# Performance work log

Measured on AMD Instinct MI355X. Metric: run time of the kernel, lower is better.

The kernel has to match this reference:

```python
import jax, jax.numpy as jnp
import numpy as np

D_MODEL = 2048
N_HEAD = 16
D_K = D_MODEL // N_HEAD  # 128
B, S = 2, 2048


def setup_inputs() -> dict:
    key = jax.random.key(0)
    ks = jax.random.split(key, 10)
    std = 1.0 / np.sqrt(D_MODEL)
    inp = {
        "x": jax.random.normal(ks[0], (B, S, D_MODEL), dtype=jnp.float32),
        "mask": jnp.ones((B, 1, S, S), dtype=jnp.int32),
        # Linear weights stored as [in, out] for x @ W + b
        "w_q": jax.random.normal(ks[1], (D_MODEL, D_MODEL), dtype=jnp.float32) * std,
        "b_q": jnp.zeros((D_MODEL,), dtype=jnp.float32),
        "w_k": jax.random.normal(ks[2], (D_MODEL, D_K), dtype=jnp.float32) * std,
        "b_k": jnp.zeros((D_K,), dtype=jnp.float32),
        "w_v": jax.random.normal(ks[3], (D_MODEL, D_K), dtype=jnp.float32) * std,
        "b_v": jnp.zeros((D_K,), dtype=jnp.float32),
        "w_o": jax.random.normal(ks[4], (D_MODEL, D_MODEL), dtype=jnp.float32) * std,
        "b_o": jnp.zeros((D_MODEL,), dtype=jnp.float32),
    }
    return inp


def reference(x, mask, w_q, b_q, w_k, b_k, w_v, b_v, w_o, b_o):
    b, s, _ = x.shape
    # Q: [b, h, s, d_k]; K/V single shared head: [b, 1, s, d_k]
    q = (x @ w_q + b_q).reshape(b, s, N_HEAD, D_K).transpose(0, 2, 1, 3)
    k = (x @ w_k + b_k)[:, None, :, :]
    v = (x @ w_v + b_v)[:, None, :, :]
    scale = jnp.sqrt(jnp.float32(D_K))
    # scores: [b, h, s, s] (K head broadcast over h)
    scores = jnp.einsum("bhqd,bzkd->bhqk", q, k) / scale
    scores = jnp.where(mask == 0, jnp.float32(-jnp.inf), scores)
    attn = jax.nn.softmax(scores, axis=-1)
    out = jnp.einsum("bhqk,bzkd->bhqd", attn, v)  # [b, h, s, d_k]
    out = out.transpose(0, 2, 1, 3).reshape(b, s, D_MODEL)
    return out @ w_o + b_o
```

## Files before the change

### kernel.cpp

```cpp
#include <hip/hip_runtime.h>

typedef __attribute__((ext_vector_type(8))) short bf16x8;
typedef __attribute__((ext_vector_type(4))) float f32x4;

#define GLD_LDS16(g, l)                                                        \
  __builtin_amdgcn_global_load_lds(                                            \
      (const __attribute__((address_space(1))) void*)(g),                      \
      (__attribute__((address_space(3))) void*)(l), 16, 0, 0)

__device__ __forceinline__ f32x4 mfma_bf16(bf16x8 a, bf16x8 b, f32x4 c) {
  return __builtin_amdgcn_mfma_f32_16x16x32_bf16(a, b, c, 0, 0, 0);
}

__device__ __forceinline__ unsigned short f2bf(float f) {
  union { float f; unsigned int u; } a;
  a.f = f;
  unsigned int u = a.u;
  unsigned int r = (u + 0x7fffu + ((u >> 16) & 1u)) >> 16;
  return (unsigned short)r;
}


__global__ void k_convert(const float* __restrict__ in,
                          unsigned short* __restrict__ out, int n8) {
  int i = blockIdx.x * 256 + threadIdx.x;
  if (i >= n8) return;
  const float4* p = reinterpret_cast<const float4*>(in) + (size_t)i * 2;
  float4 a = p[0], b = p[1];
  union { unsigned short u[8]; uint4 v; } pk;
  pk.u[0] = f2bf(a.x); pk.u[1] = f2bf(a.y); pk.u[2] = f2bf(a.z); pk.u[3] = f2bf(a.w);
  pk.u[4] = f2bf(b.x); pk.u[5] = f2bf(b.y); pk.u[6] = f2bf(b.z); pk.u[7] = f2bf(b.w);
  reinterpret_cast<uint4*>(out)[i] = pk.v;
}

__global__ void k_transpose(const float* __restrict__ in,
                            unsigned short* __restrict__ out, int R, int C) {
  __shared__ float tile[32][33];
  int c0 = blockIdx.x * 32, r0 = blockIdx.y * 32;
  int tx = threadIdx.x, ty = threadIdx.y;
#pragma unroll
  for (int j = 0; j < 4; ++j)
    tile[ty + j * 8][tx] = in[(size_t)(r0 + ty + j * 8) * C + (c0 + tx)];
  __syncthreads();
#pragma unroll
  for (int j = 0; j < 4; ++j)
    out[(size_t)(c0 + ty + j * 8) * R + (r0 + tx)] = f2bf(tile[tx][ty + j * 8]);
}

__global__ void k_bias_concat(const float* __restrict__ bq,
                              const float* __restrict__ bk,
                              const float* __restrict__ bv,
                              float* __restrict__ o) {
  int i = blockIdx.x * 256 + threadIdx.x;
  if (i < 2048) o[i] = bq[i];
  else if (i < 2176) o[i] = bk[i - 2048];
  else if (i < 2304) o[i] = bv[i - 2176];
}


template <bool OUT_F32>
__global__ __launch_bounds__(256, 2) void k_gemm(
    const unsigned short* __restrict__ A, const unsigned short* __restrict__ Bt,
    const float* __restrict__ bias, void* __restrict__ Cp, int M, int N, int K) {
  __shared__ __align__(16) unsigned short lda[128 * 32];
  __shared__ __align__(16) unsigned short ldb[128 * 32];
  const int t = threadIdx.x;
  const int l = t & 63;
  const int w = t >> 6;
  const int wr = w >> 1, wc = w & 1;
  const int lr = l & 15, lg = l >> 4;
  const int m0 = blockIdx.y * 128, n0 = blockIdx.x * 128;

  f32x4 acc[4][4] = {};

  for (int kt = 0; kt < K; kt += 32) {
#pragma unroll
    for (int c = 0; c < 2; ++c) {
      int idx = t * 8 + c * 2048;
      int row = idx >> 5, col = idx & 31;
      GLD_LDS16(A + (size_t)(m0 + row) * K + kt + col, lda + w * 512 + c * 2048);
      GLD_LDS16(Bt + (size_t)(n0 + row) * K + kt + col, ldb + w * 512 + c * 2048);
    }
    __syncthreads();
    bf16x8 af[4], bfr[4];
#pragma unroll
    for (int i = 0; i < 4; ++i)
      af[i] = *reinterpret_cast<const bf16x8*>(lda + (wr * 64 + i * 16 + lr) * 32 + lg * 8);
#pragma unroll
    for (int j = 0; j < 4; ++j)
      bfr[j] = *reinterpret_cast<const bf16x8*>(ldb + (wc * 64 + j * 16 + lr) * 32 + lg * 8);
#pragma unroll
    for (int i = 0; i < 4; ++i)
#pragma unroll
      for (int j = 0; j < 4; ++j)
        acc[i][j] = mfma_bf16(af[i], bfr[j], acc[i][j]);
    __syncthreads();
  }

#pragma unroll
  for (int j = 0; j < 4; ++j) {
    int col = n0 + wc * 64 + j * 16 + lr;
    float bv = bias[col];
#pragma unroll
    for (int i = 0; i < 4; ++i) {
      int rowb = m0 + wr * 64 + i * 16 + lg * 4;
#pragma unroll
      for (int r = 0; r < 4; ++r) {
        float v = acc[i][j][r] + bv;
        if (OUT_F32)
          reinterpret_cast<float*>(Cp)[(size_t)(rowb + r) * N + col] = v;
        else
          reinterpret_cast<unsigned short*>(Cp)[(size_t)(rowb + r) * N + col] = f2bf(v);
      }
    }
  }
}


__global__ __launch_bounds__(512, 4) void k_attn(
    const unsigned short* __restrict__ qkv, unsigned short* __restrict__ out) {
  __shared__ __align__(16) unsigned short k_lds[2][64 * 128];
  __shared__ __align__(16) unsigned short v_lds[128 * 68];
  __shared__ __align__(16) unsigned short p_lds[128 * 72];

  const int t = threadIdx.x, l = t & 63, w = t >> 6;
  const int lr = l & 15, lg = l >> 4;
  const int bid = blockIdx.x;
  const int qt = bid & 15, h = (bid >> 4) & 15, b = bid >> 8;
  const size_t rowQ0 = (size_t)b * 2048 + qt * 128;
  const size_t rowK0 = (size_t)b * 2048;

  bf16x8 qf[4];
  {
    const unsigned short* qrow = qkv + (rowQ0 + w * 16 + lr) * 2304 + h * 128;
#pragma unroll
    for (int kd = 0; kd < 4; ++kd)
      qf[kd] = *reinterpret_cast<const bf16x8*>(qrow + kd * 32 + lg * 8);
  }

#pragma unroll
  for (int c = 0; c < 2; ++c) {
    int f16 = t + c * 512;
    int row = f16 >> 4;
    int col16 = (f16 & 15) ^ (row & 7);
    GLD_LDS16(qkv + (rowK0 + row) * 2304 + 2048 + col16 * 8,
              &k_lds[0][0] + w * 512 + c * 4096);
  }
  bf16x8 vst[2];
#pragma unroll
  for (int c = 0; c < 2; ++c)
    vst[c] = *reinterpret_cast<const bf16x8*>(
        qkv + (rowK0 + l) * 2304 + 2176 + w * 16 + c * 8);
#pragma unroll
  for (int c = 0; c < 2; ++c)
#pragma unroll
    for (int e = 0; e < 8; ++e)
      v_lds[(w * 16 + c * 8 + e) * 68 + l] = (unsigned short)vst[c][e];
  __syncthreads();

  f32x4 o_acc[8] = {};
  float m_s = -1e30f, l_s = 0.f;

  const float C_SM = 0.08838834764831845f * 1.4426950408889634f;

  for (int kc = 0; kc < 32; ++kc) {
    const int cur = kc & 1;
    const unsigned short* kl = &k_lds[cur][0];

    if (kc < 31) {
#pragma unroll
      for (int c = 0; c < 2; ++c) {
        int f16 = t + c * 512;
        int row = f16 >> 4;
        int col16 = (f16 & 15) ^ (row & 7);
        GLD_LDS16(qkv + (rowK0 + (kc + 1) * 64 + row) * 2304 + 2048 + col16 * 8,
                  &k_lds[cur ^ 1][0] + w * 512 + c * 4096);
      }
#pragma unroll
      for (int c = 0; c < 2; ++c)
        vst[c] = *reinterpret_cast<const bf16x8*>(
            qkv + (rowK0 + (kc + 1) * 64 + l) * 2304 + 2176 + w * 16 + c * 8);
    }

    f32x4 sf[4];
#pragma unroll
    for (int ctK = 0; ctK < 4; ++ctK) {
      f32x4 s = {0.f, 0.f, 0.f, 0.f};
#pragma unroll
      for (int kd = 0; kd < 4; ++kd) {
        int row = ctK * 16 + lr;
        int u = (kd * 4 + lg) ^ (row & 7);
        bf16x8 kf = *reinterpret_cast<const bf16x8*>(kl + row * 128 + u * 8);
        s = mfma_bf16(kf, qf[kd], s);
      }
      sf[ctK] = s;
    }

    float vmax;
    {
      f32x4 m4 = sf[0];
#pragma unroll
      for (int ctK = 1; ctK < 4; ++ctK) {
        m4[0] = fmaxf(m4[0], sf[ctK][0]); m4[1] = fmaxf(m4[1], sf[ctK][1]);
        m4[2] = fmaxf(m4[2], sf[ctK][2]); m4[3] = fmaxf(m4[3], sf[ctK][3]);
      }
      vmax = fmaxf(fmaxf(m4[0], m4[1]), fmaxf(m4[2], m4[3]));
      vmax = fmaxf(vmax, __shfl_xor(vmax, 16));
      vmax = fmaxf(vmax, __shfl_xor(vmax, 32));
    }
    if (!__all(vmax <= m_s)) {
      float newm = fmaxf(m_s, vmax);
      float alpha = __builtin_amdgcn_exp2f((m_s - newm) * C_SM);
      m_s = newm;
      l_s *= alpha;
#pragma unroll
      for (int r = 0; r < 4; ++r) {
        float a_r = __shfl(alpha, lg * 4 + r);
#pragma unroll
        for (int ct8 = 0; ct8 < 8; ++ct8) o_acc[ct8][r] *= a_r;
      }
    }
    {
      float psum = 0.f;
#pragma unroll
      for (int ctK = 0; ctK < 4; ++ctK) {
#pragma unroll
        for (int r = 0; r < 4; ++r) {
          float p = __builtin_amdgcn_exp2f((sf[ctK][r] - m_s) * C_SM);
          sf[ctK][r] = p;
          psum += p;
        }
      }
      psum += __shfl_xor(psum, 16);
      psum += __shfl_xor(psum, 32);
      l_s += psum;
    }

#pragma unroll
    for (int ctK = 0; ctK < 4; ++ctK) {
      union { unsigned short u[4]; uint2 v; } pk;
#pragma unroll
      for (int r = 0; r < 4; ++r) pk.u[r] = f2bf(sf[ctK][r]);
      *reinterpret_cast<uint2*>(p_lds + (w * 16 + lr) * 72 + ctK * 16 + lg * 4) = pk.v;
    }

#pragma unroll
    for (int ks = 0; ks < 2; ++ks) {
      bf16x8 pf = *reinterpret_cast<const bf16x8*>(
          p_lds + (w * 16 + lr) * 72 + ks * 32 + lg * 8);
#pragma unroll
      for (int ct8 = 0; ct8 < 8; ++ct8) {
        bf16x8 vf = *reinterpret_cast<const bf16x8*>(
            v_lds + (ct8 * 16 + lr) * 68 + ks * 32 + lg * 8);
        o_acc[ct8] = mfma_bf16(pf, vf, o_acc[ct8]);
      }
    }

    __syncthreads();
    if (kc < 31) {
#pragma unroll
      for (int c = 0; c < 2; ++c)
#pragma unroll
        for (int e = 0; e < 8; ++e)
          v_lds[(w * 16 + c * 8 + e) * 68 + l] = (unsigned short)vst[c][e];
    }
    __syncthreads();
  }

  float inv = 1.0f / l_s;
  float inv4[4];
#pragma unroll
  for (int r = 0; r < 4; ++r) inv4[r] = __shfl(inv, lg * 4 + r);
#pragma unroll
  for (int r = 0; r < 4; ++r) {
    size_t row = rowQ0 + w * 16 + lg * 4 + r;
#pragma unroll
    for (int ct8 = 0; ct8 < 8; ++ct8)
      out[row * 2048 + h * 128 + ct8 * 16 + lr] = f2bf(o_acc[ct8][r] * inv4[r]);
  }
}


extern "C" void kernel_launch(void* const* d_in, const int* in_sizes, int n_in,
                              void* d_out, int out_size, void* d_ws,
                              size_t ws_size, hipStream_t stream) {
  const float* x  = (const float*)d_in[0];
  const float* wq = (const float*)d_in[2];
  const float* bq = (const float*)d_in[3];
  const float* wk = (const float*)d_in[4];
  const float* bk = (const float*)d_in[5];
  const float* wv = (const float*)d_in[6];
  const float* bv = (const float*)d_in[7];
  const float* wo = (const float*)d_in[8];
  const float* bo = (const float*)d_in[9];
  float* out = (float*)d_out;

  char* ws = (char*)d_ws;
  unsigned short* xb    = (unsigned short*)(ws);
  unsigned short* wqkvT = (unsigned short*)(ws + 16777216);
  unsigned short* woT   = (unsigned short*)(ws + 26214400);
  unsigned short* qkvb  = (unsigned short*)(ws + 34603008);
  float*          biasq = (float*)(ws + 53477376);

  k_convert<<<4096, 256, 0, stream>>>(x, xb, 1048576);
  k_transpose<<<dim3(64, 64), dim3(32, 8), 0, stream>>>(wq, wqkvT, 2048, 2048);
  k_transpose<<<dim3(4, 64),  dim3(32, 8), 0, stream>>>(wk, wqkvT + (size_t)2048 * 2048, 2048, 128);
  k_transpose<<<dim3(4, 64),  dim3(32, 8), 0, stream>>>(wv, wqkvT + (size_t)2176 * 2048, 2048, 128);
  k_transpose<<<dim3(64, 64), dim3(32, 8), 0, stream>>>(wo, woT, 2048, 2048);
  k_bias_concat<<<9, 256, 0, stream>>>(bq, bk, bv, biasq);

  k_gemm<false><<<dim3(18, 32), 256, 0, stream>>>(xb, wqkvT, biasq, qkvb, 4096, 2304, 2048);
  k_attn<<<512, 512, 0, stream>>>(qkvb, xb);
  k_gemm<true><<<dim3(16, 32), 256, 0, stream>>>(xb, woT, bo, out, 4096, 2048, 2048);
}
```

Baseline: 375.0 us.

## Double-buffer GEMM LDS, pre-transpose V, and async-load swizzled V in attention

The GEMM now double-buffers its A/B LDS tiles so the next k-tile loads while MFMAs run on the current one, dropping one barrier per iteration. A new kernel pre-transposes V into a swizzled [b, d, k] layout. Attention can then fetch V with async global-to-LDS loads into a double buffer, replacing the register staging and scalar LDS scatter that needed an extra barrier. P and V LDS layouts switch from padding to XOR swizzle, and s_setprio hints are added around the MFMA phases. The cost is an extra kernel launch, extra workspace, and more LDS per block, which may reduce occupancy.

```diff
diff --git a/kernel.cpp b/kernel.cpp
--- a/kernel.cpp
+++ b/kernel.cpp
@@ -47,6 +47,25 @@
     out[(size_t)(c0 + ty + j * 8) * R + (r0 + tx)] = f2bf(tile[tx][ty + j * 8]);
 }
 
+__global__ void k_transpose_v(const unsigned short* __restrict__ qkv,
+                              unsigned short* __restrict__ vT) {
+  __shared__ unsigned short tile[32][33];
+  int k0 = blockIdx.x * 32, d0 = blockIdx.y * 32, b = blockIdx.z;
+  int tx = threadIdx.x, ty = threadIdx.y;
+  const unsigned short* src = qkv + ((size_t)b * 2048 + k0) * 2304 + 2176 + d0;
+#pragma unroll
+  for (int j = 0; j < 4; ++j)
+    tile[ty + j * 8][tx] = src[(size_t)(ty + j * 8) * 2304 + tx];
+  __syncthreads();
+#pragma unroll
+  for (int j = 0; j < 4; ++j) {
+    int d = d0 + ty + j * 8;
+    int k = k0 + tx;
+    int ks = (k & ~63) | (((((k >> 3) & 7) ^ (d & 7)) << 3)) | (k & 7);
+    vT[(size_t)b * 262144 + (size_t)d * 2048 + ks] = tile[tx][ty + j * 8];
+  }
+}
+
 __global__ void k_bias_concat(const float* __restrict__ bq,
                               const float* __restrict__ bk,
                               const float* __restrict__ bv,
@@ -62,8 +81,8 @@
 __global__ __launch_bounds__(256, 2) void k_gemm(
     const unsigned short* __restrict__ A, const unsigned short* __restrict__ Bt,
     const float* __restrict__ bias, void* __restrict__ Cp, int M, int N, int K) {
-  __shared__ __align__(16) unsigned short lda[128 * 32];
-  __shared__ __align__(16) unsigned short ldb[128 * 32];
+  __shared__ __align__(16) unsigned short lda[2][128 * 32];
+  __shared__ __align__(16) unsigned short ldb[2][128 * 32];
   const int t = threadIdx.x;
   const int l = t & 63;
   const int w = t >> 6;
@@ -73,28 +92,54 @@
 
   f32x4 acc[4][4] = {};
 
-  for (int kt = 0; kt < K; kt += 32) {
+#pragma unroll
+  for (int c = 0; c < 2; ++c) {
+    int idx = t * 8 + c * 2048;
+    int row = idx >> 5, col = idx & 31;
+    GLD_LDS16(A + (size_t)(m0 + row) * K + col, &lda[0][0] + w * 512 + c * 2048);
+    GLD_LDS16(Bt + (size_t)(n0 + row) * K + col, &ldb[0][0] + w * 512 + c * 2048);
+  }
+  __syncthreads();
+
+  int cur = 0;
+  for (int kt = 32; kt < K; kt += 32) {
 #pragma unroll
     for (int c = 0; c < 2; ++c) {
       int idx = t * 8 + c * 2048;
       int row = idx >> 5, col = idx & 31;
-      GLD_LDS16(A + (size_t)(m0 + row) * K + kt + col, lda + w * 512 + c * 2048);
-      GLD_LDS16(Bt + (size_t)(n0 + row) * K + kt + col, ldb + w * 512 + c * 2048);
-    }
-    __syncthreads();
+      GLD_LDS16(A + (size_t)(m0 + row) * K + kt + col,
+                &lda[cur ^ 1][0] + w * 512 + c * 2048);
+      GLD_LDS16(Bt + (size_t)(n0 + row) * K + kt + col,
+                &ldb[cur ^ 1][0] + w * 512 + c * 2048);
+    }
     bf16x8 af[4], bfr[4];
 #pragma unroll
     for (int i = 0; i < 4; ++i)
-      af[i] = *reinterpret_cast<const bf16x8*>(lda + (wr * 64 + i * 16 + lr) * 32 + lg * 8);
+      af[i] = *reinterpret_cast<const bf16x8*>(&lda[cur][0] + (wr * 64 + i * 16 + lr) * 32 + lg * 8);
 #pragma unroll
     for (int j = 0; j < 4; ++j)
-      bfr[j] = *reinterpret_cast<const bf16x8*>(ldb + (wc * 64 + j * 16 + lr) * 32 + lg * 8);
+      bfr[j] = *reinterpret_cast<const bf16x8*>(&ldb[cur][0] + (wc * 64 + j * 16 + lr) * 32 + lg * 8);
 #pragma unroll
     for (int i = 0; i < 4; ++i)
 #pragma unroll
       for (int j = 0; j < 4; ++j)
         acc[i][j] = mfma_bf16(af[i], bfr[j], acc[i][j]);
     __syncthreads();
+    cur ^= 1;
+  }
+  {
+    bf16x8 af[4], bfr[4];
+#pragma unroll
+    for (int i = 0; i < 4; ++i)
+      af[i] = *reinterpret_cast<const bf16x8*>(&lda[cur][0] + (wr * 64 + i * 16 + lr) * 32 + lg * 8);
+#pragma unroll
+    for (int j = 0; j < 4; ++j)
+      bfr[j] = *reinterpret_cast<const bf16x8*>(&ldb[cur][0] + (wc * 64 + j * 16 + lr) * 32 + lg * 8);
+#pragma unroll
+    for (int i = 0; i < 4; ++i)
+#pragma unroll
+      for (int j = 0; j < 4; ++j)
+        acc[i][j] = mfma_bf16(af[i], bfr[j], acc[i][j]);
   }
 
 #pragma unroll
@@ -118,10 +163,12 @@
 
 
 __global__ __launch_bounds__(512, 4) void k_attn(
-    const unsigned short* __restrict__ qkv, unsigned short* __restrict__ out) {
+    const unsigned short* __restrict__ qkv,
+    const unsigned short* __restrict__ vT,
+    unsigned short* __restrict__ out) {
   __shared__ __align__(16) unsigned short k_lds[2][64 * 128];
-  __shared__ __align__(16) unsigned short v_lds[128 * 68];
-  __shared__ __align__(16) unsigned short p_lds[128 * 72];
+  __shared__ __align__(16) unsigned short v_lds[2][128 * 64];
+  __shared__ __align__(16) unsigned short p_lds[128 * 64];
 
   const int t = threadIdx.x, l = t & 63, w = t >> 6;
   const int lr = l & 15, lg = l >> 4;
@@ -129,6 +176,7 @@
   const int qt = bid & 15, h = (bid >> 4) & 15, b = bid >> 8;
   const size_t rowQ0 = (size_t)b * 2048 + qt * 128;
   const size_t rowK0 = (size_t)b * 2048;
+  const unsigned short* vTb = vT + (size_t)b * 262144;
 
   bf16x8 qf[4];
   {
@@ -146,16 +194,13 @@
     GLD_LDS16(qkv + (rowK0 + row) * 2304 + 2048 + col16 * 8,
               &k_lds[0][0] + w * 512 + c * 4096);
   }
-  bf16x8 vst[2];
-#pragma unroll
-  for (int c = 0; c < 2; ++c)
-    vst[c] = *reinterpret_cast<const bf16x8*>(
-        qkv + (rowK0 + l) * 2304 + 2176 + w * 16 + c * 8);
-#pragma unroll
-  for (int c = 0; c < 2; ++c)
-#pragma unroll
-    for (int e = 0; e < 8; ++e)
-      v_lds[(w * 16 + c * 8 + e) * 68 + l] = (unsigned short)vst[c][e];
+#pragma unroll
+  for (int c = 0; c < 2; ++c) {
+    int unit = t + c * 512;
+    int d = unit >> 3, u = unit & 7;
+    GLD_LDS16(vTb + (size_t)d * 2048 + u * 8,
+              &v_lds[0][0] + w * 512 + c * 4096);
+  }
   __syncthreads();
 
   f32x4 o_acc[8] = {};
@@ -166,6 +211,7 @@
   for (int kc = 0; kc < 32; ++kc) {
     const int cur = kc & 1;
     const unsigned short* kl = &k_lds[cur][0];
+    const unsigned short* vl = &v_lds[cur][0];
 
     if (kc < 31) {
 #pragma unroll
@@ -177,12 +223,16 @@
                   &k_lds[cur ^ 1][0] + w * 512 + c * 4096);
       }
 #pragma unroll
-      for (int c = 0; c < 2; ++c)
-        vst[c] = *reinterpret_cast<const bf16x8*>(
-            qkv + (rowK0 + (kc + 1) * 64 + l) * 2304 + 2176 + w * 16 + c * 8);
+      for (int c = 0; c < 2; ++c) {
+        int unit = t + c * 512;
+        int d = unit >> 3, u = unit & 7;
+        GLD_LDS16(vTb + (size_t)d * 2048 + (kc + 1) * 64 + u * 8,
+                  &v_lds[cur ^ 1][0] + w * 512 + c * 4096);
+      }
     }
 
     f32x4 sf[4];
+    __builtin_amdgcn_s_setprio(1);
 #pragma unroll
     for (int ctK = 0; ctK < 4; ++ctK) {
       f32x4 s = {0.f, 0.f, 0.f, 0.f};
@@ -195,6 +245,7 @@
       }
       sf[ctK] = s;
     }
+    __builtin_amdgcn_s_setprio(0);
 
     float vmax;
     {
@@ -241,29 +292,24 @@
       union { unsigned short u[4]; uint2 v; } pk;
 #pragma unroll
       for (int r = 0; r < 4; ++r) pk.u[r] = f2bf(sf[ctK][r]);
-      *reinterpret_cast<uint2*>(p_lds + (w * 16 + lr) * 72 + ctK * 16 + lg * 4) = pk.v;
-    }
-
+      *reinterpret_cast<uint2*>(
+          p_lds + (w * 16 + lr) * 64 + ((ctK * 16 + lg * 4) ^ ((lr & 7) << 3))) = pk.v;
+    }
+
+    __builtin_amdgcn_s_setprio(1);
 #pragma unroll
     for (int ks = 0; ks < 2; ++ks) {
       bf16x8 pf = *reinterpret_cast<const bf16x8*>(
-          p_lds + (w * 16 + lr) * 72 + ks * 32 + lg * 8);
+          p_lds + (w * 16 + lr) * 64 + ((ks * 32 + lg * 8) ^ ((lr & 7) << 3)));
 #pragma unroll
       for (int ct8 = 0; ct8 < 8; ++ct8) {
         bf16x8 vf = *reinterpret_cast<const bf16x8*>(
-            v_lds + (ct8 * 16 + lr) * 68 + ks * 32 + lg * 8);
+            vl + (ct8 * 16 + lr) * 64 + (((ks * 4 + lg) ^ (lr & 7)) * 8));
         o_acc[ct8] = mfma_bf16(pf, vf, o_acc[ct8]);
       }
     }
-
-    __syncthreads();
-    if (kc < 31) {
-#pragma unroll
-      for (int c = 0; c < 2; ++c)
-#pragma unroll
-        for (int e = 0; e < 8; ++e)
-          v_lds[(w * 16 + c * 8 + e) * 68 + l] = (unsigned short)vst[c][e];
-    }
+    __builtin_amdgcn_s_setprio(0);
+
     __syncthreads();
   }
 
@@ -301,6 +347,7 @@
   unsigned short* woT   = (unsigned short*)(ws + 26214400);
   unsigned short* qkvb  = (unsigned short*)(ws + 34603008);
   float*          biasq = (float*)(ws + 53477376);
+  unsigned short* vTb   = (unsigned short*)(ws + 53486592);
 
   k_convert<<<4096, 256, 0, stream>>>(x, xb, 1048576);
   k_transpose<<<dim3(64, 64), dim3(32, 8), 0, stream>>>(wq, wqkvT, 2048, 2048);
@@ -310,6 +357,7 @@
   k_bias_concat<<<9, 256, 0, stream>>>(bq, bk, bv, biasq);
 
   k_gemm<false><<<dim3(18, 32), 256, 0, stream>>>(xb, wqkvT, biasq, qkvb, 4096, 2304, 2048);
-  k_attn<<<512, 512, 0, stream>>>(qkvb, xb);
+  k_transpose_v<<<dim3(64, 4, 2), dim3(32, 8), 0, stream>>>(qkvb, vTb);
+  k_attn<<<512, 512, 0, stream>>>(qkvb, vTb, xb);
   k_gemm<true><<<dim3(16, 32), 256, 0, stream>>>(xb, woT, bo, out, 4096, 2048, 2048);
 }
```

New measurement: 362.8 us. 1.03x faster.
